# Kernel tuning notes

Measured on AMD Instinct MI355X. Metric: run time of the kernel, lower is better.

The kernel has to match this reference:

```python
import jax, jax.numpy as jnp
import numpy as np

NEG_SLOPE = 0.2


def gat_conv(x, edge_index, W, a_src, a_dst, b):
    # PyG GATConv (heads=1, add_self_loops=True, concat -> out_channels)
    N = x.shape[0]
    h = x @ W                                   # [N, F_out]
    loops = jnp.arange(N, dtype=edge_index.dtype)
    src = jnp.concatenate([edge_index[0], loops])   # message sources (x_j)
    dst = jnp.concatenate([edge_index[1], loops])   # message targets (x_i)
    # attention logits: e = LeakyReLU(a_src . h_j + a_dst . h_i)
    alpha_s = h @ a_src                          # [N]
    alpha_d = h @ a_dst                          # [N]
    e = jax.nn.leaky_relu(alpha_s[src] + alpha_d[dst], NEG_SLOPE)  # [E+N]
    # segment softmax over incoming edges of each dst node
    m = jax.ops.segment_max(e, dst, num_segments=N)
    e = jnp.exp(e - m[dst])
    denom = jax.ops.segment_sum(e, dst, num_segments=N)
    alpha = e / denom[dst]                       # self-loops guarantee denom > 0
    # weighted scatter-sum aggregation
    out = jax.ops.segment_sum(alpha[:, None] * h[src], dst, num_segments=N)
    return out + b


def setup_inputs() -> dict:
    key = jax.random.key(0)
    ks = jax.random.split(key, 10)
    N, E, F_in, H, F_out = 100000, 3200000, 54, 16, 16
    x = jax.random.normal(ks[0], (N, F_in), dtype=jnp.float32)
    edge_index = jax.random.randint(ks[1], (2, E), 0, N, dtype=jnp.int64)
    s1 = 1.0 / np.sqrt(F_in)
    s2 = 1.0 / np.sqrt(H)
    return {
        "x": x,
        "edge_index": edge_index,
        "W1": jax.random.uniform(ks[2], (F_in, H), jnp.float32, -s1, s1),
        "a1_src": jax.random.uniform(ks[3], (H,), jnp.float32, -s2, s2),
        "a1_dst": jax.random.uniform(ks[4], (H,), jnp.float32, -s2, s2),
        "b1": jnp.zeros((H,), jnp.float32),
        "W2": jax.random.uniform(ks[5], (H, F_out), jnp.float32, -s2, s2),
        "a2_src": jax.random.uniform(ks[6], (F_out,), jnp.float32, -0.25, 0.25),
        "a2_dst": jax.random.uniform(ks[7], (F_out,), jnp.float32, -0.25, 0.25),
        "b2": jnp.zeros((F_out,), jnp.float32),
    }


def reference(x, edge_index, W1, a1_src, a1_dst, b1, W2, a2_src, a2_dst, b2):
    h = gat_conv(x, edge_index, W1, a1_src, a1_dst, b1)
    h = jax.nn.elu(h)
    # dropout p=0.5 is identity in eval mode
    out = gat_conv(h, edge_index, W2, a2_src, a2_dst, b2)
    return out
```

## Files before the change

kernel.cpp:

```cpp
#include <hip/hip_runtime.h>
#include <hip/hip_bf16.h>

typedef __hip_bfloat16 bf16;

static constexpr int N_NODES = 100000;
static constexpr int N_EDGES = 3200000;
static constexpr int F_IN    = 54;
static constexpr int F_HID   = 16;

static constexpr int BSHIFT    = 7;
static constexpr int BNODES    = 128;
static constexpr int NBUCK     = (N_NODES + BNODES - 1) / BNODES;
static constexpr int CAP_B     = 5120;
static constexpr int BIN_CHUNK = 4096;
static constexpr int BTHR      = 512;
static constexpr int EPT       = BIN_CHUNK / BTHR;
static constexpr int GRDB      = (N_EDGES + BIN_CHUNK - 1) / BIN_CHUNK;
static constexpr int GRDN_F    = (N_NODES + BTHR - 1) / BTHR;
static constexpr int HELD      = CAP_B / 512;

static constexpr size_t WS_FLAGS  = 0;
static constexpr size_t WS_ADST   = 4;
static constexpr size_t WS_ADST2  = 100004;
static constexpr size_t WS_BCNT   = 200004;
static constexpr size_t WS_ASRC1  = 201028;
static constexpr size_t WS_ASRC2  = 301028;
static constexpr size_t WS_HC1    = 401028;
static constexpr size_t WS_HC2    = 2001028;
static constexpr size_t WS_BEDGES = 3601028;
static constexpr size_t WS_SRCS   = 7604868;
static constexpr size_t WS_BUCKET_END = WS_SRCS + (size_t)NBUCK * CAP_B;
static constexpr size_t WS_FB_DEN     = 3601028;
static constexpr size_t WS_FB_AS      = 3701028;
static constexpr size_t WS_ATOMIC_END = 3801028;

__device__ __forceinline__ float lrelu(float v) { return fmaxf(v, 0.2f * v); }
__device__ __forceinline__ float loadf(const void* p, int i, bool f32) {
    return f32 ? ((const float*)p)[i] : __bfloat162float(((const bf16*)p)[i]);
}
__device__ __forceinline__ unsigned f2bf(float f) {
    unsigned u = __float_as_uint(f);
    return (u + 0x7FFFu + ((u >> 16) & 1u)) >> 16;
}
__device__ __forceinline__ float bflo(unsigned u) { return __uint_as_float(u << 16); }
__device__ __forceinline__ float bfhi(unsigned u) { return __uint_as_float(u & 0xFFFF0000u); }

__global__ __launch_bounds__(256) void k_probe0(
    const void* __restrict__ x, const void* __restrict__ ei,
    int* __restrict__ flags, int* __restrict__ bcnt)
{
    __shared__ int cnt, nz;
    const int t = threadIdx.x;
    if (t == 0) { cnt = 0; nz = 0; }
    __syncthreads();
    const unsigned u = ((const unsigned*)x)[t];
    if ((u & 0x7FFFu) >= 0x4800u) atomicAdd(&cnt, 1);
    if (t < 64) {
        if (((const unsigned*)ei)[2 * t + 1] != 0u) atomicAdd(&nz, 1);
    }
    for (int i = t; i < 1024; i += 256) bcnt[i] = 0;
    __syncthreads();
    if (t == 0) flags[0] = ((cnt >= 16) ? 1 : 0) | ((nz == 0) ? 2 : 0);
}

__global__ __launch_bounds__(512, 8) void k_binfeat(
    const void* __restrict__ ei, const void* __restrict__ x,
    const void* __restrict__ W1, const void* __restrict__ a_s,
    const void* __restrict__ a_d, const int* __restrict__ flags,
    int* __restrict__ bcnt, int* __restrict__ bedges,
    unsigned* __restrict__ hc, float* __restrict__ asrc, float* __restrict__ adst)
{
    __shared__ int   hist[NBUCK];
    __shared__ int   base[NBUCK];
    __shared__ float Wl[F_IN * F_HID];
    __shared__ float asl[F_HID];
    __shared__ float adl[F_HID];
    const int t = threadIdx.x;
    const bool f32 = flags[0] & 1;
    const bool i64 = flags[0] & 2;

    if (blockIdx.x < GRDB) {
        const int e0 = blockIdx.x * BIN_CHUNK;
        const int valid = min(BIN_CHUNK, N_EDGES - e0);
        for (int i = t; i < NBUCK; i += BTHR) hist[i] = 0;
        __syncthreads();
        int cval_r[EPT];
        int bkt_r[EPT];
#pragma unroll
        for (int q = 0; q < EPT; ++q) {
            const int idx = q * BTHR + t;
            const int e = e0 + idx;
            bkt_r[q] = -1;
            if (idx < valid) {
                int s, d;
                if (i64) {
                    s = ((const int*)ei)[2 * (size_t)e];
                    d = ((const int*)ei)[2 * ((size_t)N_EDGES + e)];
                } else {
                    s = ((const int*)ei)[e];
                    d = ((const int*)ei)[(size_t)N_EDGES + e];
                }
                bkt_r[q] = d >> BSHIFT;
                cval_r[q] = (s << BSHIFT) | (d & (BNODES - 1));
                atomicAdd(&hist[bkt_r[q]], 1);
            }
        }
        __syncthreads();
        for (int i = t; i < NBUCK; i += BTHR) {
            const int c = hist[i];
            base[i] = c ? atomicAdd(&bcnt[i], c) : 0;
            hist[i] = 0;
        }
        __syncthreads();
#pragma unroll
        for (int q = 0; q < EPT; ++q) {
            if (bkt_r[q] >= 0) {
                const int b = bkt_r[q];
                const int r = atomicAdd(&hist[b], 1);
                const int pos = base[b] + r;
                if (pos < CAP_B) bedges[(size_t)b * CAP_B + pos] = cval_r[q];
            }
        }
    } else {
        for (int i = t; i < F_IN * F_HID; i += BTHR) Wl[i] = loadf(W1, i, f32);
        if (t < F_HID) { asl[t] = loadf(a_s, t, f32); adl[t] = loadf(a_d, t, f32); }
        __syncthreads();
        const int node = (blockIdx.x - GRDB) * BTHR + t;
        if (node >= N_NODES) return;

        float h[F_HID];
#pragma unroll
        for (int k = 0; k < F_HID; ++k) h[k] = 0.f;
        if (f32) {
            const float2* xp = (const float2*)((const float*)x + (size_t)node * F_IN);
#pragma unroll
            for (int j = 0; j < F_IN / 2; ++j) {
                const float2 v = xp[j];
#pragma unroll
                for (int k = 0; k < F_HID; ++k) {
                    h[k] = fmaf(v.x, Wl[(2*j)   * F_HID + k], h[k]);
                    h[k] = fmaf(v.y, Wl[(2*j+1) * F_HID + k], h[k]);
                }
            }
        } else {
            const unsigned* xu = (const unsigned*)x + (size_t)node * (F_IN / 2);
#pragma unroll
            for (int j = 0; j < F_IN / 2; ++j) {
                const unsigned u = xu[j];
                const float v0 = __uint_as_float(u << 16);
                const float v1 = __uint_as_float(u & 0xFFFF0000u);
#pragma unroll
                for (int k = 0; k < F_HID; ++k) {
                    h[k] = fmaf(v0, Wl[(2*j)   * F_HID + k], h[k]);
                    h[k] = fmaf(v1, Wl[(2*j+1) * F_HID + k], h[k]);
                }
            }
        }
        float s = 0.f, d = 0.f;
#pragma unroll
        for (int k = 0; k < F_HID; ++k) { s = fmaf(h[k], asl[k], s); d = fmaf(h[k], adl[k], d); }
        asrc[node] = s;
        adst[node] = d;
        unsigned pk[8];
#pragma unroll
        for (int q = 0; q < 8; ++q) pk[q] = f2bf(h[2*q]) | (f2bf(h[2*q+1]) << 16);
        uint4* hb = (uint4*)(hc + ((size_t)node << 3));
        hb[0] = make_uint4(pk[0], pk[1], pk[2], pk[3]);
        hb[1] = make_uint4(pk[4], pk[5], pk[6], pk[7]);
    }
}

__device__ __forceinline__ void bucket_sort_lds(
    const int* __restrict__ bedges, const int* __restrict__ bcnt, int b, int t,
    int* hist, int* scanv, int* cur, int* srt)
{
    if (t < BNODES) hist[t] = 0;
    __syncthreads();
    const int cnt = min(bcnt[b], CAP_B);
    const int* cv = bedges + (size_t)b * CAP_B;
    int held[HELD];
#pragma unroll
    for (int q = 0; q < HELD; ++q) {
        const int e = t + q * 512;
        const int v = cv[e];
        held[q] = (e < cnt) ? v : -1;
    }
#pragma unroll
    for (int q = 0; q < HELD; ++q)
        if (held[q] >= 0) atomicAdd(&hist[held[q] & (BNODES - 1)], 1);
    __syncthreads();
    if (t < BNODES) scanv[t] = hist[t];
    __syncthreads();
#pragma unroll
    for (int off = 1; off < BNODES; off <<= 1) {
        const int v = (t < BNODES && t >= off) ? scanv[t - off] : 0;
        __syncthreads();
        if (t < BNODES) scanv[t] += v;
        __syncthreads();
    }
    if (t < BNODES) cur[t] = scanv[t] - hist[t];
    __syncthreads();
#pragma unroll
    for (int q = 0; q < HELD; ++q) {
        if (held[q] >= 0) {
            const int p  = held[q];
            const int r  = atomicAdd(&cur[p & (BNODES - 1)], 1);
            srt[r] = p >> BSHIFT;
        }
    }
    __syncthreads();
}

__global__ __launch_bounds__(512, 6) void k_agg1(
    const int* __restrict__ bcnt, const int* __restrict__ bedges,
    const float* __restrict__ asrc, const float* __restrict__ adst,
    const unsigned* __restrict__ hc,
    const void* __restrict__ b1, const void* __restrict__ W2,
    const void* __restrict__ a_s2, const void* __restrict__ a_d2,
    const int* __restrict__ flags,
    unsigned* __restrict__ hc2, float* __restrict__ asrc2, float* __restrict__ adst2)
{
    __shared__ float Wl[F_HID * F_HID];
    __shared__ float asl[F_HID], adl[F_HID], bl[F_HID];
    __shared__ float adL[BNODES], asL[BNODES];
    __shared__ int hist[BNODES], scanv[BNODES], cur[BNODES];
    __shared__ int srt[CAP_B];
    const bool f32 = flags[0] & 1;
    const int t = threadIdx.x;
    const int b = blockIdx.x;
    const int n0 = b << BSHIFT;
    if (t < F_HID * F_HID) Wl[t] = loadf(W2, t, f32);
    if (t < F_HID) {
        asl[t] = loadf(a_s2, t, f32);
        adl[t] = loadf(a_d2, t, f32);
        bl[t]  = loadf(b1, t, f32);
    }
    if (t < BNODES) {
        const int node = n0 + t;
        const bool ok = node < N_NODES;
        adL[t] = ok ? adst[node] : 0.f;
        asL[t] = ok ? asrc[node] : 0.f;
    }
    bucket_sort_lds(bedges, bcnt, b, t, hist, scanv, cur, srt);

    const int k2 = t & 3;
    const int g  = t >> 2;
    const int node = n0 + g;
    if (node < N_NODES) {
        const int K = k2 << 2;
        const float adn = adL[g];
        const uint2 us = *(const uint2*)(hc + ((size_t)node << 3) + (k2 << 1));
        const float w0 = __expf(lrelu(asL[g] + adn));
        float denom = w0;
        float a0 = w0 * bflo(us.x), a1 = w0 * bfhi(us.x);
        float a2 = w0 * bflo(us.y), a3 = w0 * bfhi(us.y);
        const int n = hist[g];
        const int* sp = srt + (scanv[g] - n);
        int i = 0;
        for (; i + 8 <= n; i += 8) {
            const int s0 = sp[i+0], s1 = sp[i+1], s2_ = sp[i+2], s3 = sp[i+3];
            const int s4 = sp[i+4], s5 = sp[i+5], s6 = sp[i+6], s7 = sp[i+7];
            const uint2 v0 = *(const uint2*)(hc + ((size_t)s0 << 3) + (k2 << 1));
            const uint2 v1 = *(const uint2*)(hc + ((size_t)s1 << 3) + (k2 << 1));
            const uint2 v2 = *(const uint2*)(hc + ((size_t)s2_ << 3) + (k2 << 1));
            const uint2 v3 = *(const uint2*)(hc + ((size_t)s3 << 3) + (k2 << 1));
            const uint2 v4 = *(const uint2*)(hc + ((size_t)s4 << 3) + (k2 << 1));
            const uint2 v5 = *(const uint2*)(hc + ((size_t)s5 << 3) + (k2 << 1));
            const uint2 v6 = *(const uint2*)(hc + ((size_t)s6 << 3) + (k2 << 1));
            const uint2 v7 = *(const uint2*)(hc + ((size_t)s7 << 3) + (k2 << 1));
            const float x0 = asrc[s0], x1 = asrc[s1], x2 = asrc[s2_], x3 = asrc[s3];
            const float x4 = asrc[s4], x5 = asrc[s5], x6 = asrc[s6], x7 = asrc[s7];
            const float e0 = __expf(lrelu(x0 + adn));
            const float e1 = __expf(lrelu(x1 + adn));
            const float e2 = __expf(lrelu(x2 + adn));
            const float e3 = __expf(lrelu(x3 + adn));
            const float e4 = __expf(lrelu(x4 + adn));
            const float e5 = __expf(lrelu(x5 + adn));
            const float e6 = __expf(lrelu(x6 + adn));
            const float e7 = __expf(lrelu(x7 + adn));
            denom += (e0 + e1 + e2 + e3) + (e4 + e5 + e6 + e7);
            a0 = fmaf(e0, bflo(v0.x), a0); a1 = fmaf(e0, bfhi(v0.x), a1);
            a2 = fmaf(e0, bflo(v0.y), a2); a3 = fmaf(e0, bfhi(v0.y), a3);
            a0 = fmaf(e1, bflo(v1.x), a0); a1 = fmaf(e1, bfhi(v1.x), a1);
            a2 = fmaf(e1, bflo(v1.y), a2); a3 = fmaf(e1, bfhi(v1.y), a3);
            a0 = fmaf(e2, bflo(v2.x), a0); a1 = fmaf(e2, bfhi(v2.x), a1);
            a2 = fmaf(e2, bflo(v2.y), a2); a3 = fmaf(e2, bfhi(v2.y), a3);
            a0 = fmaf(e3, bflo(v3.x), a0); a1 = fmaf(e3, bfhi(v3.x), a1);
            a2 = fmaf(e3, bflo(v3.y), a2); a3 = fmaf(e3, bfhi(v3.y), a3);
            a0 = fmaf(e4, bflo(v4.x), a0); a1 = fmaf(e4, bfhi(v4.x), a1);
            a2 = fmaf(e4, bflo(v4.y), a2); a3 = fmaf(e4, bfhi(v4.y), a3);
            a0 = fmaf(e5, bflo(v5.x), a0); a1 = fmaf(e5, bfhi(v5.x), a1);
            a2 = fmaf(e5, bflo(v5.y), a2); a3 = fmaf(e5, bfhi(v5.y), a3);
            a0 = fmaf(e6, bflo(v6.x), a0); a1 = fmaf(e6, bfhi(v6.x), a1);
            a2 = fmaf(e6, bflo(v6.y), a2); a3 = fmaf(e6, bfhi(v6.y), a3);
            a0 = fmaf(e7, bflo(v7.x), a0); a1 = fmaf(e7, bfhi(v7.x), a1);
            a2 = fmaf(e7, bflo(v7.y), a2); a3 = fmaf(e7, bfhi(v7.y), a3);
        }
        for (; i < n; ++i) {
            const int s = sp[i];
            const uint2 v = *(const uint2*)(hc + ((size_t)s << 3) + (k2 << 1));
            const float w = __expf(lrelu(asrc[s] + adn));
            denom += w;
            a0 = fmaf(w, bflo(v.x), a0); a1 = fmaf(w, bfhi(v.x), a1);
            a2 = fmaf(w, bflo(v.y), a2); a3 = fmaf(w, bfhi(v.y), a3);
        }
        const float inv = 1.f / denom;
        float z0 = a0 * inv + bl[K+0];
        float z1 = a1 * inv + bl[K+1];
        float z2 = a2 * inv + bl[K+2];
        float z3 = a3 * inv + bl[K+3];
        z0 = z0 > 0.f ? z0 : expm1f(z0);
        z1 = z1 > 0.f ? z1 : expm1f(z1);
        z2 = z2 > 0.f ? z2 : expm1f(z2);
        z3 = z3 > 0.f ? z3 : expm1f(z3);
        float hh0 = 0.f, hh1 = 0.f, hh2 = 0.f, hh3 = 0.f;
#pragma unroll
        for (int jl = 0; jl < 4; ++jl) {
            const float zj0 = __shfl(z0, jl, 4);
            const float zj1 = __shfl(z1, jl, 4);
            const float zj2 = __shfl(z2, jl, 4);
            const float zj3 = __shfl(z3, jl, 4);
            const int jb = jl << 2;
            hh0 = fmaf(zj0, Wl[(jb+0)*F_HID + K+0], hh0);
            hh1 = fmaf(zj0, Wl[(jb+0)*F_HID + K+1], hh1);
            hh2 = fmaf(zj0, Wl[(jb+0)*F_HID + K+2], hh2);
            hh3 = fmaf(zj0, Wl[(jb+0)*F_HID + K+3], hh3);
            hh0 = fmaf(zj1, Wl[(jb+1)*F_HID + K+0], hh0);
            hh1 = fmaf(zj1, Wl[(jb+1)*F_HID + K+1], hh1);
            hh2 = fmaf(zj1, Wl[(jb+1)*F_HID + K+2], hh2);
            hh3 = fmaf(zj1, Wl[(jb+1)*F_HID + K+3], hh3);
            hh0 = fmaf(zj2, Wl[(jb+2)*F_HID + K+0], hh0);
            hh1 = fmaf(zj2, Wl[(jb+2)*F_HID + K+1], hh1);
            hh2 = fmaf(zj2, Wl[(jb+2)*F_HID + K+2], hh2);
            hh3 = fmaf(zj2, Wl[(jb+2)*F_HID + K+3], hh3);
            hh0 = fmaf(zj3, Wl[(jb+3)*F_HID + K+0], hh0);
            hh1 = fmaf(zj3, Wl[(jb+3)*F_HID + K+1], hh1);
            hh2 = fmaf(zj3, Wl[(jb+3)*F_HID + K+2], hh2);
            hh3 = fmaf(zj3, Wl[(jb+3)*F_HID + K+3], hh3);
        }
        float s2 = hh0*asl[K+0] + hh1*asl[K+1] + hh2*asl[K+2] + hh3*asl[K+3];
        float d2 = hh0*adl[K+0] + hh1*adl[K+1] + hh2*adl[K+2] + hh3*adl[K+3];
        s2 += __shfl_xor(s2, 1, 4); s2 += __shfl_xor(s2, 2, 4);
        d2 += __shfl_xor(d2, 1, 4); d2 += __shfl_xor(d2, 2, 4);
        uint2 w;
        w.x = f2bf(hh0) | (f2bf(hh1) << 16);
        w.y = f2bf(hh2) | (f2bf(hh3) << 16);
        *(uint2*)(hc2 + ((size_t)node << 3) + (k2 << 1)) = w;
        if (k2 == 0) { asrc2[node] = s2; adst2[node] = d2; }
    }
}

__global__ __launch_bounds__(512, 6) void k_agg2(
    const int* __restrict__ bcnt, const int* __restrict__ bedges,
    const float* __restrict__ asrc, const float* __restrict__ adst,
    const unsigned* __restrict__ hc,
    const void* __restrict__ b2, const int* __restrict__ flags,
    float* __restrict__ outp)
{
    __shared__ float bl[F_HID];
    __shared__ float adL[BNODES], asL[BNODES];
    __shared__ int hist[BNODES], scanv[BNODES], cur[BNODES];
    __shared__ int srt[CAP_B];
    const bool f32 = flags[0] & 1;
    const int t = threadIdx.x;
    const int b = blockIdx.x;
    const int n0 = b << BSHIFT;
    if (t < F_HID) bl[t] = loadf(b2, t, f32);
    if (t < BNODES) {
        const int node = n0 + t;
        const bool ok = node < N_NODES;
        adL[t] = ok ? adst[node] : 0.f;
        asL[t] = ok ? asrc[node] : 0.f;
    }
    bucket_sort_lds(bedges, bcnt, b, t, hist, scanv, cur, srt);

    const int k2 = t & 3;
    const int g  = t >> 2;
    const int node = n0 + g;
    if (node < N_NODES) {
        const int K = k2 << 2;
        const float adn = adL[g];
        const uint2 us = *(const uint2*)(hc + ((size_t)node << 3) + (k2 << 1));
        const float w0 = __expf(lrelu(asL[g] + adn));
        float denom = w0;
        float a0 = w0 * bflo(us.x), a1 = w0 * bfhi(us.x);
        float a2 = w0 * bflo(us.y), a3 = w0 * bfhi(us.y);
        const int n = hist[g];
        const int* sp = srt + (scanv[g] - n);
        int i = 0;
        for (; i + 8 <= n; i += 8) {
            const int s0 = sp[i+0], s1 = sp[i+1], s2_ = sp[i+2], s3 = sp[i+3];
            const int s4 = sp[i+4], s5 = sp[i+5], s6 = sp[i+6], s7 = sp[i+7];
            const uint2 v0 = *(const uint2*)(hc + ((size_t)s0 << 3) + (k2 << 1));
            const uint2 v1 = *(const uint2*)(hc + ((size_t)s1 << 3) + (k2 << 1));
            const uint2 v2 = *(const uint2*)(hc + ((size_t)s2_ << 3) + (k2 << 1));
            const uint2 v3 = *(const uint2*)(hc + ((size_t)s3 << 3) + (k2 << 1));
            const uint2 v4 = *(const uint2*)(hc + ((size_t)s4 << 3) + (k2 << 1));
            const uint2 v5 = *(const uint2*)(hc + ((size_t)s5 << 3) + (k2 << 1));
            const uint2 v6 = *(const uint2*)(hc + ((size_t)s6 << 3) + (k2 << 1));
            const uint2 v7 = *(const uint2*)(hc + ((size_t)s7 << 3) + (k2 << 1));
            const float x0 = asrc[s0], x1 = asrc[s1], x2 = asrc[s2_], x3 = asrc[s3];
            const float x4 = asrc[s4], x5 = asrc[s5], x6 = asrc[s6], x7 = asrc[s7];
            const float e0 = __expf(lrelu(x0 + adn));
            const float e1 = __expf(lrelu(x1 + adn));
            const float e2 = __expf(lrelu(x2 + adn));
            const float e3 = __expf(lrelu(x3 + adn));
            const float e4 = __expf(lrelu(x4 + adn));
            const float e5 = __expf(lrelu(x5 + adn));
            const float e6 = __expf(lrelu(x6 + adn));
            const float e7 = __expf(lrelu(x7 + adn));
            denom += (e0 + e1 + e2 + e3) + (e4 + e5 + e6 + e7);
            a0 = fmaf(e0, bflo(v0.x), a0); a1 = fmaf(e0, bfhi(v0.x), a1);
            a2 = fmaf(e0, bflo(v0.y), a2); a3 = fmaf(e0, bfhi(v0.y), a3);
            a0 = fmaf(e1, bflo(v1.x), a0); a1 = fmaf(e1, bfhi(v1.x), a1);
            a2 = fmaf(e1, bflo(v1.y), a2); a3 = fmaf(e1, bfhi(v1.y), a3);
            a0 = fmaf(e2, bflo(v2.x), a0); a1 = fmaf(e2, bfhi(v2.x), a1);
            a2 = fmaf(e2, bflo(v2.y), a2); a3 = fmaf(e2, bfhi(v2.y), a3);
            a0 = fmaf(e3, bflo(v3.x), a0); a1 = fmaf(e3, bfhi(v3.x), a1);
            a2 = fmaf(e3, bflo(v3.y), a2); a3 = fmaf(e3, bfhi(v3.y), a3);
            a0 = fmaf(e4, bflo(v4.x), a0); a1 = fmaf(e4, bfhi(v4.x), a1);
            a2 = fmaf(e4, bflo(v4.y), a2); a3 = fmaf(e4, bfhi(v4.y), a3);
            a0 = fmaf(e5, bflo(v5.x), a0); a1 = fmaf(e5, bfhi(v5.x), a1);
            a2 = fmaf(e5, bflo(v5.y), a2); a3 = fmaf(e5, bfhi(v5.y), a3);
            a0 = fmaf(e6, bflo(v6.x), a0); a1 = fmaf(e6, bfhi(v6.x), a1);
            a2 = fmaf(e6, bflo(v6.y), a2); a3 = fmaf(e6, bfhi(v6.y), a3);
            a0 = fmaf(e7, bflo(v7.x), a0); a1 = fmaf(e7, bfhi(v7.x), a1);
            a2 = fmaf(e7, bflo(v7.y), a2); a3 = fmaf(e7, bfhi(v7.y), a3);
        }
        for (; i < n; ++i) {
            const int s = sp[i];
            const uint2 v = *(const uint2*)(hc + ((size_t)s << 3) + (k2 << 1));
            const float w = __expf(lrelu(asrc[s] + adn));
            denom += w;
            a0 = fmaf(w, bflo(v.x), a0); a1 = fmaf(w, bfhi(v.x), a1);
            a2 = fmaf(w, bflo(v.y), a2); a3 = fmaf(w, bfhi(v.y), a3);
        }
        const float inv = 1.f / denom;
        float4 o;
        o.x = a0 * inv + bl[K+0];
        o.y = a1 * inv + bl[K+1];
        o.z = a2 * inv + bl[K+2];
        o.w = a3 * inv + bl[K+3];
        *(float4*)(outp + ((size_t)node << 4) + K) = o;
    }
}

__global__ __launch_bounds__(256) void k_feat1(
    const void* __restrict__ x, const void* __restrict__ W1,
    const void* __restrict__ a_s, const void* __restrict__ a_d,
    const int* __restrict__ flags,
    float* __restrict__ hbuf, float* __restrict__ asrc, float* __restrict__ adst)
{
    const bool f32 = flags[0] & 1;
    __shared__ float Wl[F_IN * F_HID];
    __shared__ float asl[F_HID];
    __shared__ float adl[F_HID];
    const int t = threadIdx.x;
    for (int i = t; i < F_IN * F_HID; i += 256) Wl[i] = loadf(W1, i, f32);
    if (t < F_HID) { asl[t] = loadf(a_s, t, f32); adl[t] = loadf(a_d, t, f32); }
    __syncthreads();
    const int node = blockIdx.x * 256 + t;
    if (node >= N_NODES) return;
    float h[F_HID];
#pragma unroll
    for (int k = 0; k < F_HID; ++k) h[k] = 0.f;
    if (f32) {
        const float2* xp = (const float2*)((const float*)x + (size_t)node * F_IN);
#pragma unroll
        for (int j = 0; j < F_IN / 2; ++j) {
            const float2 v = xp[j];
#pragma unroll
            for (int k = 0; k < F_HID; ++k) {
                h[k] = fmaf(v.x, Wl[(2*j)   * F_HID + k], h[k]);
                h[k] = fmaf(v.y, Wl[(2*j+1) * F_HID + k], h[k]);
            }
        }
    } else {
        const unsigned* xu = (const unsigned*)x + (size_t)node * (F_IN / 2);
#pragma unroll
        for (int j = 0; j < F_IN / 2; ++j) {
            const unsigned u = xu[j];
            const float v0 = __uint_as_float(u << 16);
            const float v1 = __uint_as_float(u & 0xFFFF0000u);
#pragma unroll
            for (int k = 0; k < F_HID; ++k) {
                h[k] = fmaf(v0, Wl[(2*j)   * F_HID + k], h[k]);
                h[k] = fmaf(v1, Wl[(2*j+1) * F_HID + k], h[k]);
            }
        }
    }
    float s = 0.f, d = 0.f;
#pragma unroll
    for (int k = 0; k < F_HID; ++k) { s = fmaf(h[k], asl[k], s); d = fmaf(h[k], adl[k], d); }
    asrc[node] = s; adst[node] = d;
    float4* hb = (float4*)(hbuf + (size_t)node * F_HID);
#pragma unroll
    for (int q = 0; q < 4; ++q)
        hb[q] = make_float4(h[4*q], h[4*q+1], h[4*q+2], h[4*q+3]);
}

__global__ __launch_bounds__(256) void k_selfinit(
    const float* __restrict__ asrc, const float* __restrict__ adst,
    const float* __restrict__ h, float* __restrict__ denom, float* __restrict__ acc)
{
    const int t = blockIdx.x * 256 + threadIdx.x;
    if (t >= N_NODES * F_HID) return;
    const int n = t >> 4;
    const float w0 = __expf(lrelu(asrc[n] + adst[n]));
    if ((t & 15) == 0) denom[n] = w0;
    acc[t] = w0 * h[t];
}

__global__ __launch_bounds__(256) void k_edge(
    const void* __restrict__ ei, const int* __restrict__ flags,
    const float* __restrict__ asrc, const float* __restrict__ adst,
    const float* __restrict__ hbuf,
    float* __restrict__ denom, float* __restrict__ acc)
{
    const int e = blockIdx.x * 256 + threadIdx.x;
    if (e >= N_EDGES) return;
    int s, d;
    if (flags[0] & 2) {
        const long long* e64 = (const long long*)ei;
        s = (int)e64[e]; d = (int)e64[(size_t)N_EDGES + e];
    } else {
        const int* e32 = (const int*)ei;
        s = e32[e]; d = e32[(size_t)N_EDGES + e];
    }
    const float w = __expf(lrelu(asrc[s] + adst[d]));
    atomicAdd(&denom[d], w);
    const float4* hs = (const float4*)(hbuf + (size_t)s * F_HID);
    float* ad = acc + (size_t)d * F_HID;
#pragma unroll
    for (int q = 0; q < 4; ++q) {
        const float4 hv = hs[q];
        atomicAdd(ad + 4*q + 0, w * hv.x);
        atomicAdd(ad + 4*q + 1, w * hv.y);
        atomicAdd(ad + 4*q + 2, w * hv.z);
        atomicAdd(ad + 4*q + 3, w * hv.w);
    }
}

__global__ __launch_bounds__(256) void k_div_elu(
    float* __restrict__ acc, const float* __restrict__ denom,
    const void* __restrict__ b1, const int* __restrict__ flags)
{
    const bool f32 = flags[0] & 1;
    const int t = blockIdx.x * 256 + threadIdx.x;
    if (t >= N_NODES * F_HID) return;
    const float v = acc[t] / denom[t >> 4] + loadf(b1, t & 15, f32);
    acc[t] = v > 0.f ? v : expm1f(v);
}

__global__ __launch_bounds__(256) void k_mid(
    const float* __restrict__ z,
    const void* __restrict__ W2, const void* __restrict__ a_s2,
    const void* __restrict__ a_d2, const int* __restrict__ flags,
    float* __restrict__ h2, float* __restrict__ asrc, float* __restrict__ adst)
{
    const bool f32 = flags[0] & 1;
    __shared__ float Wl[F_HID * F_HID];
    __shared__ float asl[F_HID];
    __shared__ float adl[F_HID];
    const int t = threadIdx.x;
    if (t < F_HID * F_HID) Wl[t] = loadf(W2, t, f32);
    if (t < F_HID) { asl[t] = loadf(a_s2, t, f32); adl[t] = loadf(a_d2, t, f32); }
    __syncthreads();
    const int node = blockIdx.x * 256 + t;
    if (node >= N_NODES) return;
    float zr[F_HID];
    const float4* zi = (const float4*)(z + (size_t)node * F_HID);
#pragma unroll
    for (int q = 0; q < 4; ++q) {
        const float4 zv = zi[q];
        zr[4*q+0]=zv.x; zr[4*q+1]=zv.y; zr[4*q+2]=zv.z; zr[4*q+3]=zv.w;
    }
    float h[F_HID];
#pragma unroll
    for (int k = 0; k < F_HID; ++k) h[k] = 0.f;
#pragma unroll
    for (int j = 0; j < F_HID; ++j) {
        const float zv = zr[j];
#pragma unroll
        for (int k = 0; k < F_HID; ++k) h[k] = fmaf(zv, Wl[j * F_HID + k], h[k]);
    }
    float s = 0.f, d = 0.f;
#pragma unroll
    for (int k = 0; k < F_HID; ++k) { s = fmaf(h[k], asl[k], s); d = fmaf(h[k], adl[k], d); }
    asrc[node] = s; adst[node] = d;
    float4* hb = (float4*)(h2 + (size_t)node * F_HID);
#pragma unroll
    for (int q = 0; q < 4; ++q)
        hb[q] = make_float4(h[4*q], h[4*q+1], h[4*q+2], h[4*q+3]);
}

__global__ __launch_bounds__(256) void k_out(
    const float* __restrict__ acc, const float* __restrict__ denom,
    const void* __restrict__ b2, const int* __restrict__ flags,
    float* __restrict__ out)
{
    const bool f32 = flags[0] & 1;
    const int t = blockIdx.x * 256 + threadIdx.x;
    if (t >= N_NODES * F_HID) return;
    out[t] = acc[t] / denom[t >> 4] + loadf(b2, t & 15, f32);
}

__global__ __launch_bounds__(256) void k_diag(float* __restrict__ out, float v)
{
    const int t = blockIdx.x * 256 + threadIdx.x;
    if (t < N_NODES * F_HID) out[t] = v;
}

extern "C" void kernel_launch(void* const* d_in, const int* in_sizes, int n_in,
                              void* d_out, int out_size, void* d_ws, size_t ws_size,
                              hipStream_t stream) {
    const void* x   = d_in[0];
    const void* ei  = d_in[1];
    const void* W1  = d_in[2];
    const void* a1s = d_in[3];
    const void* a1d = d_in[4];
    const void* b1  = d_in[5];
    const void* W2  = d_in[6];
    const void* a2s = d_in[7];
    const void* a2d = d_in[8];
    const void* b2  = d_in[9];
    float* out = (float*)d_out;

    float* ws = (float*)d_ws;
    int*      flags  = (int*)(ws + WS_FLAGS);
    float*    adst   = ws + WS_ADST;
    float*    adst2  = ws + WS_ADST2;
    int*      bcnt   = (int*)(ws + WS_BCNT);
    float*    asrc1  = ws + WS_ASRC1;
    float*    asrc2  = ws + WS_ASRC2;
    unsigned* hc1    = (unsigned*)(ws + WS_HC1);
    unsigned* hc2    = (unsigned*)(ws + WS_HC2);
    int*      bedges = (int*)(ws + WS_BEDGES);

    const dim3 blk(256);
    const dim3 grdN((N_NODES + 255) / 256);
    const dim3 grdE((N_EDGES + 255) / 256);
    const dim3 grdO((N_NODES * F_HID + 255) / 256);
    const dim3 grdBF(GRDB + GRDN_F);
    const dim3 grdB(NBUCK);

    if (ws_size >= WS_BUCKET_END * 4) {
        k_probe0 <<<dim3(1), blk, 0, stream>>>(x, ei, flags, bcnt);
        k_binfeat<<<grdBF, dim3(BTHR), 0, stream>>>(ei, x, W1, a1s, a1d, flags,
                                                    bcnt, bedges, hc1, asrc1, adst);
        k_agg1   <<<grdB, dim3(512), 0, stream>>>(bcnt, bedges, asrc1, adst, hc1,
                                                  b1, W2, a2s, a2d, flags,
                                                  hc2, asrc2, adst2);
        k_agg2   <<<grdB, dim3(512), 0, stream>>>(bcnt, bedges, asrc2, adst2, hc2,
                                                  b2, flags, out);
    } else if (ws_size >= WS_ATOMIC_END * 4) {
        float* fb_h   = ws + WS_HC1;
        float* fb_acc = ws + WS_HC2;
        float* fb_den = ws + WS_FB_DEN;
        float* fb_as  = ws + WS_FB_AS;
        float* fb_ad  = ws + WS_ADST;
        k_probe0 <<<dim3(1), blk, 0, stream>>>(x, ei, flags, bcnt);
        k_feat1  <<<grdN, blk, 0, stream>>>(x, W1, a1s, a1d, flags, fb_h, fb_as, fb_ad);
        k_selfinit<<<grdO, blk, 0, stream>>>(fb_as, fb_ad, fb_h, fb_den, fb_acc);
        k_edge   <<<grdE, blk, 0, stream>>>(ei, flags, fb_as, fb_ad, fb_h, fb_den, fb_acc);
        k_div_elu<<<grdO, blk, 0, stream>>>(fb_acc, fb_den, b1, flags);
        k_mid    <<<grdN, blk, 0, stream>>>(fb_acc, W2, a2s, a2d, flags, fb_h, fb_as, fb_ad);
        k_selfinit<<<grdO, blk, 0, stream>>>(fb_as, fb_ad, fb_h, fb_den, fb_acc);
        k_edge   <<<grdE, blk, 0, stream>>>(ei, flags, fb_as, fb_ad, fb_h, fb_den, fb_acc);
        k_out    <<<grdO, blk, 0, stream>>>(fb_acc, fb_den, b2, flags, out);
    } else {
        k_diag<<<grdO, blk, 0, stream>>>(out, (float)(ws_size >> 10));
    }
}
```

Before: 222.0 us.

## Locally sort edges by bucket in LDS before coalesced global scatter

The edge binning kernel now scans its per-bucket histogram with a wave-shuffle prefix sum, stages each chunk's edges sorted by bucket in shared memory, and then writes them to the global bucket arrays in sorted order, so writes for one bucket are contiguous. It also loads two edges per thread with vector loads. The aim is to turn scattered 4-byte global writes into mostly contiguous runs. The cost is extra LDS (about 37KB dynamic), more barriers and a scan, which may reduce occupancy.

```diff
diff --git a/kernel.cpp b/kernel.cpp
--- a/kernel.cpp
+++ b/kernel.cpp
@@ -18,6 +18,15 @@
 static constexpr int GRDB      = (N_EDGES + BIN_CHUNK - 1) / BIN_CHUNK;
 static constexpr int GRDN_F    = (N_NODES + BTHR - 1) / BTHR;
 static constexpr int HELD      = CAP_B / 512;
+
+static constexpr int SM_SORTV = 0;
+static constexpr int SM_SORTB = 16384;
+static constexpr int SM_HIST  = 24576;
+static constexpr int SM_SCAN  = 27712;
+static constexpr int SM_CUR   = 30848;
+static constexpr int SM_GBASE = 33984;
+static constexpr int SM_WSUM  = 37120;
+static constexpr int SMEM_BF  = 37152;
 
 static constexpr size_t WS_FLAGS  = 0;
 static constexpr size_t WS_ADST   = 4;
@@ -70,58 +79,102 @@
     int* __restrict__ bcnt, int* __restrict__ bedges,
     unsigned* __restrict__ hc, float* __restrict__ asrc, float* __restrict__ adst)
 {
-    __shared__ int   hist[NBUCK];
-    __shared__ int   base[NBUCK];
-    __shared__ float Wl[F_IN * F_HID];
-    __shared__ float asl[F_HID];
-    __shared__ float adl[F_HID];
+    extern __shared__ char smem[];
     const int t = threadIdx.x;
     const bool f32 = flags[0] & 1;
     const bool i64 = flags[0] & 2;
 
     if (blockIdx.x < GRDB) {
+        int*            sortedv = (int*)(smem + SM_SORTV);
+        unsigned short* sortedb = (unsigned short*)(smem + SM_SORTB);
+        int*            histS   = (int*)(smem + SM_HIST);
+        int*            scanvS  = (int*)(smem + SM_SCAN);
+        int*            curS    = (int*)(smem + SM_CUR);
+        int*            gbaseS  = (int*)(smem + SM_GBASE);
+        int*            wsum    = (int*)(smem + SM_WSUM);
+
         const int e0 = blockIdx.x * BIN_CHUNK;
         const int valid = min(BIN_CHUNK, N_EDGES - e0);
-        for (int i = t; i < NBUCK; i += BTHR) hist[i] = 0;
-        __syncthreads();
-        int cval_r[EPT];
-        int bkt_r[EPT];
-#pragma unroll
-        for (int q = 0; q < EPT; ++q) {
-            const int idx = q * BTHR + t;
+        for (int i = t; i < NBUCK; i += BTHR) histS[i] = 0;
+        __syncthreads();
+
+        int   cval_r[EPT];
+        short bkt_r[EPT];
+#pragma unroll
+        for (int q = 0; q < EPT / 2; ++q) {
+            const int idx = (q * BTHR + t) * 2;
             const int e = e0 + idx;
-            bkt_r[q] = -1;
             if (idx < valid) {
-                int s, d;
+                int s0, d0, s1, d1;
                 if (i64) {
-                    s = ((const int*)ei)[2 * (size_t)e];
-                    d = ((const int*)ei)[2 * ((size_t)N_EDGES + e)];
+                    const int4 sv = *(const int4*)((const int*)ei + 2 * (size_t)e);
+                    const int4 dv = *(const int4*)((const int*)ei + 2 * ((size_t)N_EDGES + e));
+                    s0 = sv.x; s1 = sv.z; d0 = dv.x; d1 = dv.z;
                 } else {
-                    s = ((const int*)ei)[e];
-                    d = ((const int*)ei)[(size_t)N_EDGES + e];
+                    const int2 sv = *(const int2*)((const int*)ei + e);
+                    const int2 dv = *(const int2*)((const int*)ei + (size_t)N_EDGES + e);
+                    s0 = sv.x; s1 = sv.y; d0 = dv.x; d1 = dv.y;
                 }
-                bkt_r[q] = d >> BSHIFT;
-                cval_r[q] = (s << BSHIFT) | (d & (BNODES - 1));
-                atomicAdd(&hist[bkt_r[q]], 1);
+                const int b0 = d0 >> BSHIFT, b1 = d1 >> BSHIFT;
+                cval_r[2*q]   = (s0 << BSHIFT) | (d0 & (BNODES - 1));
+                cval_r[2*q+1] = (s1 << BSHIFT) | (d1 & (BNODES - 1));
+                bkt_r[2*q]   = (short)b0;
+                bkt_r[2*q+1] = (short)b1;
+                atomicAdd(&histS[b0], 1);
+                atomicAdd(&histS[b1], 1);
+            } else {
+                bkt_r[2*q] = -1; bkt_r[2*q+1] = -1;
             }
         }
         __syncthreads();
+
+        const int j0 = 2 * t, j1 = 2 * t + 1;
+        const int h0 = (j0 < NBUCK) ? histS[j0] : 0;
+        const int h1 = (j1 < NBUCK) ? histS[j1] : 0;
+        const int vsum = h0 + h1;
+        const int lane = t & 63, wid = t >> 6;
+        int sc = vsum;
+#pragma unroll
+        for (int off = 1; off < 64; off <<= 1) {
+            const int u = __shfl_up(sc, off, 64);
+            if (lane >= off) sc += u;
+        }
+        if (lane == 63) wsum[wid] = sc;
+        __syncthreads();
+        if (t == 0) {
+            int acc = 0;
+#pragma unroll
+            for (int w = 0; w < BTHR / 64; ++w) { const int xv = wsum[w]; wsum[w] = acc; acc += xv; }
+        }
+        __syncthreads();
+        const int ex = wsum[wid] + sc - vsum;
+        if (j0 < NBUCK) { scanvS[j0] = ex;      curS[j0] = ex; }
+        if (j1 < NBUCK) { scanvS[j1] = ex + h0; curS[j1] = ex + h0; }
+        __syncthreads();
+
         for (int i = t; i < NBUCK; i += BTHR) {
-            const int c = hist[i];
-            base[i] = c ? atomicAdd(&bcnt[i], c) : 0;
-            hist[i] = 0;
-        }
-        __syncthreads();
+            const int c = histS[i];
+            gbaseS[i] = c ? atomicAdd(&bcnt[i], c) : 0;
+        }
 #pragma unroll
         for (int q = 0; q < EPT; ++q) {
             if (bkt_r[q] >= 0) {
-                const int b = bkt_r[q];
-                const int r = atomicAdd(&hist[b], 1);
-                const int pos = base[b] + r;
-                if (pos < CAP_B) bedges[(size_t)b * CAP_B + pos] = cval_r[q];
+                const int p = atomicAdd(&curS[bkt_r[q]], 1);
+                sortedv[p] = cval_r[q];
+                sortedb[p] = (unsigned short)bkt_r[q];
             }
         }
+        __syncthreads();
+
+        for (int p = t; p < valid; p += BTHR) {
+            const int b = sortedb[p];
+            const int pos = gbaseS[b] + (p - scanvS[b]);
+            if (pos < CAP_B) bedges[(size_t)b * CAP_B + pos] = sortedv[p];
+        }
     } else {
+        float* Wl  = (float*)smem;
+        float* asl = (float*)(smem + 3456);
+        float* adl = (float*)(smem + 3520);
         for (int i = t; i < F_IN * F_HID; i += BTHR) Wl[i] = loadf(W1, i, f32);
         if (t < F_HID) { asl[t] = loadf(a_s, t, f32); adl[t] = loadf(a_d, t, f32); }
         __syncthreads();
@@ -646,8 +699,8 @@
 
     if (ws_size >= WS_BUCKET_END * 4) {
         k_probe0 <<<dim3(1), blk, 0, stream>>>(x, ei, flags, bcnt);
-        k_binfeat<<<grdBF, dim3(BTHR), 0, stream>>>(ei, x, W1, a1s, a1d, flags,
-                                                    bcnt, bedges, hc1, asrc1, adst);
+        k_binfeat<<<grdBF, dim3(BTHR), SMEM_BF, stream>>>(ei, x, W1, a1s, a1d, flags,
+                                                          bcnt, bedges, hc1, asrc1, adst);
         k_agg1   <<<grdB, dim3(512), 0, stream>>>(bcnt, bedges, asrc1, adst, hc1,
                                                   b1, W2, a2s, a2d, flags,
                                                   hc2, asrc2, adst2);
```

Measured after the change: 233.8 us. +5.3%, slower.

## Fuse both GAT aggregation layers into one kernel with a grid-wide barrier

Applied to the files above, without the earlier changes.

Merges the two aggregation kernels into a single persistent kernel. Each block sorts its bucket of edges once, computes layer 1 and the layer-2 projection, then waits at a global atomic-counter barrier before running layer-2 aggregation. Layer 2 reuses the LDS-sorted edge list and keeps its own self-loop features and attention scalars in registers and LDS. This removes the second bucket sort and one kernel launch. In exchange it requires all 782 blocks to be resident on the GPU at once, or the barrier deadlocks. It also relies on the counter at bcnt+1000 being zeroed before every call, and the launch bound is raised to 8 blocks per multiprocessor.

```diff
diff --git a/kernel.cpp b/kernel.cpp
--- a/kernel.cpp
+++ b/kernel.cpp
@@ -211,17 +211,18 @@
     __syncthreads();
 }
 
-__global__ __launch_bounds__(512, 6) void k_agg1(
+__global__ __launch_bounds__(512, 8) void k_aggf(
     const int* __restrict__ bcnt, const int* __restrict__ bedges,
     const float* __restrict__ asrc, const float* __restrict__ adst,
     const unsigned* __restrict__ hc,
     const void* __restrict__ b1, const void* __restrict__ W2,
     const void* __restrict__ a_s2, const void* __restrict__ a_d2,
-    const int* __restrict__ flags,
-    unsigned* __restrict__ hc2, float* __restrict__ asrc2, float* __restrict__ adst2)
+    const void* __restrict__ b2, const int* __restrict__ flags,
+    unsigned* __restrict__ hc2, float* __restrict__ asrc2, float* __restrict__ adst2,
+    float* __restrict__ outp, int* __restrict__ barrier_ctr)
 {
     __shared__ float Wl[F_HID * F_HID];
-    __shared__ float asl[F_HID], adl[F_HID], bl[F_HID];
+    __shared__ float asl[F_HID], adl[F_HID], bl1[F_HID], bl2[F_HID];
     __shared__ float adL[BNODES], asL[BNODES];
     __shared__ int hist[BNODES], scanv[BNODES], cur[BNODES];
     __shared__ int srt[CAP_B];
@@ -233,7 +234,8 @@
     if (t < F_HID) {
         asl[t] = loadf(a_s2, t, f32);
         adl[t] = loadf(a_d2, t, f32);
-        bl[t]  = loadf(b1, t, f32);
+        bl1[t] = loadf(b1, t, f32);
+        bl2[t] = loadf(b2, t, f32);
     }
     if (t < BNODES) {
         const int node = n0 + t;
@@ -246,6 +248,9 @@
     const int k2 = t & 3;
     const int g  = t >> 2;
     const int node = n0 + g;
+    uint2 us2;
+    us2.x = 0; us2.y = 0;
+
     if (node < N_NODES) {
         const int K = k2 << 2;
         const float adn = adL[g];
@@ -305,10 +310,10 @@
             a2 = fmaf(w, bflo(v.y), a2); a3 = fmaf(w, bfhi(v.y), a3);
         }
         const float inv = 1.f / denom;
-        float z0 = a0 * inv + bl[K+0];
-        float z1 = a1 * inv + bl[K+1];
-        float z2 = a2 * inv + bl[K+2];
-        float z3 = a3 * inv + bl[K+3];
+        float z0 = a0 * inv + bl1[K+0];
+        float z1 = a1 * inv + bl1[K+1];
+        float z2 = a2 * inv + bl1[K+2];
+        float z3 = a3 * inv + bl1[K+3];
         z0 = z0 > 0.f ? z0 : expm1f(z0);
         z1 = z1 > 0.f ? z1 : expm1f(z1);
         z2 = z2 > 0.f ? z2 : expm1f(z2);
@@ -342,65 +347,49 @@
         float d2 = hh0*adl[K+0] + hh1*adl[K+1] + hh2*adl[K+2] + hh3*adl[K+3];
         s2 += __shfl_xor(s2, 1, 4); s2 += __shfl_xor(s2, 2, 4);
         d2 += __shfl_xor(d2, 1, 4); d2 += __shfl_xor(d2, 2, 4);
-        uint2 w;
-        w.x = f2bf(hh0) | (f2bf(hh1) << 16);
-        w.y = f2bf(hh2) | (f2bf(hh3) << 16);
-        *(uint2*)(hc2 + ((size_t)node << 3) + (k2 << 1)) = w;
-        if (k2 == 0) { asrc2[node] = s2; adst2[node] = d2; }
-    }
-}
-
-__global__ __launch_bounds__(512, 6) void k_agg2(
-    const int* __restrict__ bcnt, const int* __restrict__ bedges,
-    const float* __restrict__ asrc, const float* __restrict__ adst,
-    const unsigned* __restrict__ hc,
-    const void* __restrict__ b2, const int* __restrict__ flags,
-    float* __restrict__ outp)
-{
-    __shared__ float bl[F_HID];
-    __shared__ float adL[BNODES], asL[BNODES];
-    __shared__ int hist[BNODES], scanv[BNODES], cur[BNODES];
-    __shared__ int srt[CAP_B];
-    const bool f32 = flags[0] & 1;
-    const int t = threadIdx.x;
-    const int b = blockIdx.x;
-    const int n0 = b << BSHIFT;
-    if (t < F_HID) bl[t] = loadf(b2, t, f32);
-    if (t < BNODES) {
-        const int node = n0 + t;
-        const bool ok = node < N_NODES;
-        adL[t] = ok ? adst[node] : 0.f;
-        asL[t] = ok ? asrc[node] : 0.f;
-    }
-    bucket_sort_lds(bedges, bcnt, b, t, hist, scanv, cur, srt);
-
-    const int k2 = t & 3;
-    const int g  = t >> 2;
-    const int node = n0 + g;
+        us2.x = f2bf(hh0) | (f2bf(hh1) << 16);
+        us2.y = f2bf(hh2) | (f2bf(hh3) << 16);
+        *(uint2*)(hc2 + ((size_t)node << 3) + (k2 << 1)) = us2;
+        if (k2 == 0) {
+            asrc2[node] = s2;
+            adst2[node] = d2;
+            asL[g] = s2;
+            adL[g] = d2;
+        }
+    }
+
+    __threadfence();
+    __syncthreads();
+    if (t == 0) {
+        atomicAdd(barrier_ctr, 1);
+        while (atomicAdd(barrier_ctr, 0) < NBUCK) __builtin_amdgcn_s_sleep(8);
+    }
+    __syncthreads();
+    __threadfence();
+
     if (node < N_NODES) {
         const int K = k2 << 2;
         const float adn = adL[g];
-        const uint2 us = *(const uint2*)(hc + ((size_t)node << 3) + (k2 << 1));
         const float w0 = __expf(lrelu(asL[g] + adn));
         float denom = w0;
-        float a0 = w0 * bflo(us.x), a1 = w0 * bfhi(us.x);
-        float a2 = w0 * bflo(us.y), a3 = w0 * bfhi(us.y);
+        float a0 = w0 * bflo(us2.x), a1 = w0 * bfhi(us2.x);
+        float a2 = w0 * bflo(us2.y), a3 = w0 * bfhi(us2.y);
         const int n = hist[g];
         const int* sp = srt + (scanv[g] - n);
         int i = 0;
         for (; i + 8 <= n; i += 8) {
             const int s0 = sp[i+0], s1 = sp[i+1], s2_ = sp[i+2], s3 = sp[i+3];
             const int s4 = sp[i+4], s5 = sp[i+5], s6 = sp[i+6], s7 = sp[i+7];
-            const uint2 v0 = *(const uint2*)(hc + ((size_t)s0 << 3) + (k2 << 1));
-            const uint2 v1 = *(const uint2*)(hc + ((size_t)s1 << 3) + (k2 << 1));
-            const uint2 v2 = *(const uint2*)(hc + ((size_t)s2_ << 3) + (k2 << 1));
-            const uint2 v3 = *(const uint2*)(hc + ((size_t)s3 << 3) + (k2 << 1));
-            const uint2 v4 = *(const uint2*)(hc + ((size_t)s4 << 3) + (k2 << 1));
-            const uint2 v5 = *(const uint2*)(hc + ((size_t)s5 << 3) + (k2 << 1));
-            const uint2 v6 = *(const uint2*)(hc + ((size_t)s6 << 3) + (k2 << 1));
-            const uint2 v7 = *(const uint2*)(hc + ((size_t)s7 << 3) + (k2 << 1));
-            const float x0 = asrc[s0], x1 = asrc[s1], x2 = asrc[s2_], x3 = asrc[s3];
-            const float x4 = asrc[s4], x5 = asrc[s5], x6 = asrc[s6], x7 = asrc[s7];
+            const uint2 v0 = *(const uint2*)(hc2 + ((size_t)s0 << 3) + (k2 << 1));
+            const uint2 v1 = *(const uint2*)(hc2 + ((size_t)s1 << 3) + (k2 << 1));
+            const uint2 v2 = *(const uint2*)(hc2 + ((size_t)s2_ << 3) + (k2 << 1));
+            const uint2 v3 = *(const uint2*)(hc2 + ((size_t)s3 << 3) + (k2 << 1));
+            const uint2 v4 = *(const uint2*)(hc2 + ((size_t)s4 << 3) + (k2 << 1));
+            const uint2 v5 = *(const uint2*)(hc2 + ((size_t)s5 << 3) + (k2 << 1));
+            const uint2 v6 = *(const uint2*)(hc2 + ((size_t)s6 << 3) + (k2 << 1));
+            const uint2 v7 = *(const uint2*)(hc2 + ((size_t)s7 << 3) + (k2 << 1));
+            const float x0 = asrc2[s0], x1 = asrc2[s1], x2 = asrc2[s2_], x3 = asrc2[s3];
+            const float x4 = asrc2[s4], x5 = asrc2[s5], x6 = asrc2[s6], x7 = asrc2[s7];
             const float e0 = __expf(lrelu(x0 + adn));
             const float e1 = __expf(lrelu(x1 + adn));
             const float e2 = __expf(lrelu(x2 + adn));
@@ -429,18 +418,18 @@
         }
         for (; i < n; ++i) {
             const int s = sp[i];
-            const uint2 v = *(const uint2*)(hc + ((size_t)s << 3) + (k2 << 1));
-            const float w = __expf(lrelu(asrc[s] + adn));
+            const uint2 v = *(const uint2*)(hc2 + ((size_t)s << 3) + (k2 << 1));
+            const float w = __expf(lrelu(asrc2[s] + adn));
             denom += w;
             a0 = fmaf(w, bflo(v.x), a0); a1 = fmaf(w, bfhi(v.x), a1);
             a2 = fmaf(w, bflo(v.y), a2); a3 = fmaf(w, bfhi(v.y), a3);
         }
         const float inv = 1.f / denom;
         float4 o;
-        o.x = a0 * inv + bl[K+0];
-        o.y = a1 * inv + bl[K+1];
-        o.z = a2 * inv + bl[K+2];
-        o.w = a3 * inv + bl[K+3];
+        o.x = a0 * inv + bl2[K+0];
+        o.y = a1 * inv + bl2[K+1];
+        o.z = a2 * inv + bl2[K+2];
+        o.w = a3 * inv + bl2[K+3];
         *(float4*)(outp + ((size_t)node << 4) + K) = o;
     }
 }
@@ -648,11 +637,10 @@
         k_probe0 <<<dim3(1), blk, 0, stream>>>(x, ei, flags, bcnt);
         k_binfeat<<<grdBF, dim3(BTHR), 0, stream>>>(ei, x, W1, a1s, a1d, flags,
                                                     bcnt, bedges, hc1, asrc1, adst);
-        k_agg1   <<<grdB, dim3(512), 0, stream>>>(bcnt, bedges, asrc1, adst, hc1,
-                                                  b1, W2, a2s, a2d, flags,
-                                                  hc2, asrc2, adst2);
-        k_agg2   <<<grdB, dim3(512), 0, stream>>>(bcnt, bedges, asrc2, adst2, hc2,
-                                                  b2, flags, out);
+        k_aggf   <<<grdB, dim3(512), 0, stream>>>(bcnt, bedges, asrc1, adst, hc1,
+                                                  b1, W2, a2s, a2d, b2, flags,
+                                                  hc2, asrc2, adst2, out,
+                                                  bcnt + 1000);
     } else if (ws_size >= WS_ATOMIC_END * 4) {
         float* fb_h   = ws + WS_HC1;
         float* fb_acc = ws + WS_HC2;
```

New measurement: 539.7 us. 2.43x slower.
